# Kernel optimization log

Hardware: AMD Instinct MI355X
Metric: run time of the kernel (lower is better)

The kernel has to match this reference:

```python
import jax, jax.numpy as jnp
import numpy as np

B, C, H, W = 4, 256, 64, 64
EMB = C // 8  # embedding_channels = inChannels // k


def _conv1x1(x, w, b):
    # x: [B, Cin, H, W], w: [Cout, Cin], b: [Cout] -> [B, Cout, H, W]
    return jnp.einsum('oi,bihw->bohw', w, x) + b[None, :, None, None]


def setup_inputs() -> dict:
    key = jax.random.key(0)
    ks = jax.random.split(key, 10)
    s = 0.05
    return {
        'x': jax.random.normal(ks[0], (B, C, H, W), dtype=jnp.float32),
        'key_w': jax.random.normal(ks[1], (EMB, C), dtype=jnp.float32) * s,
        'key_b': jax.random.normal(ks[2], (EMB,), dtype=jnp.float32) * s,
        'query_w': jax.random.normal(ks[3], (EMB, C), dtype=jnp.float32) * s,
        'query_b': jax.random.normal(ks[4], (EMB,), dtype=jnp.float32) * s,
        'value_w': jax.random.normal(ks[5], (EMB, C), dtype=jnp.float32) * s,
        'value_b': jax.random.normal(ks[6], (EMB,), dtype=jnp.float32) * s,
        'att_w': jax.random.normal(ks[7], (C, EMB), dtype=jnp.float32) * s,
        'att_b': jax.random.normal(ks[8], (C,), dtype=jnp.float32) * s,
        'gamma': jnp.zeros((), dtype=jnp.float32),
    }


def reference(x, key_w, key_b, query_w, query_b, value_w, value_b, att_w, att_b, gamma):
    b, c, h, w = x.shape
    n = h * w
    f = _conv1x1(x, key_w, key_b).reshape(b, -1, n)    # [B, E, N]
    g = _conv1x1(x, query_w, query_b).reshape(b, -1, n)  # [B, E, N]
    hh = _conv1x1(x, value_w, value_b).reshape(b, -1, n)  # [B, E, N]
    # s[b,i,j] = sum_e f[b,e,i] * g[b,e,j]
    s = jnp.einsum('bei,bej->bij', f, g)  # [B, N, N]
    # NOTE: softmax over dim=1 (the i / key-index axis), NOT the last dim
    beta = jax.nn.softmax(s, axis=1)
    v = jnp.einsum('bei,bij->bej', hh, beta).reshape(b, -1, h, w)  # [B, E, H, W]
    o = _conv1x1(v, att_w, att_b)  # [B, C, H, W]
    y = gamma * o + x
    return (y, o)
```

## Files before the change

### kernel.cpp

```cpp
#include <hip/hip_runtime.h>
#include <hip/hip_bf16.h>
#include <math.h>

#define BB 4
#define CC 256
#define NN 4096
#define EE 32

typedef __attribute__((ext_vector_type(8))) short bf16x8;
typedef __attribute__((ext_vector_type(4))) float f32x4;
typedef __attribute__((ext_vector_type(16))) float f32x16;
typedef __attribute__((ext_vector_type(2))) unsigned uint32x2_t;

__device__ inline unsigned short f2bf(float x) {
    union { __hip_bfloat16 h; unsigned short u; } cv;
    cv.h = __float2bfloat16(x);
    return cv.u;
}
__device__ inline unsigned pk2(float lo, float hi) {
    return ((unsigned)f2bf(hi) << 16) | (unsigned)f2bf(lo);
}
__device__ inline float fexp2(float x) { return __builtin_amdgcn_exp2f(x); }
__device__ inline unsigned cvtpk(float lo, float hi) {
    unsigned r;
    asm("v_cvt_pk_bf16_f32 %0, %1, %2" : "=v"(r) : "v"(lo), "v"(hi));
    return r;
}
__device__ inline float bflo(unsigned u) {
    union { unsigned v; float f; } c; c.v = u << 16; return c.f;
}
__device__ inline float bfhi(unsigned u) {
    union { unsigned v; float f; } c; c.v = u & 0xFFFF0000u; return c.f;
}

__global__ __launch_bounds__(256) void wcvt_kernel(
    const float* __restrict__ kw, const float* __restrict__ kb,
    const float* __restrict__ qw, const float* __restrict__ qb,
    const float* __restrict__ vw, const float* __restrict__ vb,
    __hip_bfloat16* __restrict__ wB, float* __restrict__ bB)
{
    int r = blockIdx.x;
    int t = threadIdx.x;
    int rr = r & 31;
    const float* src; float scale = 1.f;
    if (r < 32)      src = kw;
    else if (r < 64) { src = qw; scale = 1.44269504f; }
    else             src = vw;
    if (t < 64) {
        float4 v = *(const float4*)(src + rr * 256 + t * 4);
        uint2 p;
        p.x = pk2(v.x * scale, v.y * scale);
        p.y = pk2(v.z * scale, v.w * scale);
        *(uint2*)((unsigned short*)wB + r * 256 + t * 4) = p;
    }
    if (r == 0 && t >= 64 && t < 160) {
        int e = t - 64;
        const float* bs = (e < 32) ? kb : ((e < 64) ? qb : vb);
        float sc = (e >= 32 && e < 64) ? 1.44269504f : 1.f;
        bB[e] = bs[e & 31] * sc;
    }
}

__global__ __launch_bounds__(256) void proj_kernel(
    const float* __restrict__ x,
    const __hip_bfloat16* __restrict__ wB, const float* __restrict__ bB,
    __hip_bfloat16* __restrict__ fT, __hip_bfloat16* __restrict__ gT,
    __hip_bfloat16* __restrict__ hT)
{
    __shared__ unsigned xs[32][132];
    int b     = blockIdx.x >> 7;
    int ibase = (blockIdx.x & 127) << 5;

    int t   = threadIdx.x;
    int ig4 = (t & 7) * 4;
    int crw = t >> 3;
    const float* xb = x + (size_t)b * CC * NN + ibase;
#pragma unroll
    for (int it = 0; it < 4; ++it) {
        int cp = it * 32 + crw;
        float4 fa = *(const float4*)(xb + (size_t)(2 * cp) * NN + ig4);
        float4 fc = *(const float4*)(xb + (size_t)(2 * cp + 1) * NN + ig4);
        xs[ig4 + 0][cp] = pk2(fa.x, fc.x);
        xs[ig4 + 1][cp] = pk2(fa.y, fc.y);
        xs[ig4 + 2][cp] = pk2(fa.z, fc.z);
        xs[ig4 + 3][cp] = pk2(fa.w, fc.w);
    }
    __syncthreads();

    int wv = threadIdx.x >> 6;
    int l  = threadIdx.x & 63;
    int q15  = l & 15, g = l >> 4;
    int isub = wv & 1, eh = wv >> 1;
    int irow = (isub << 4) + q15;
    const __hip_bfloat16* w0 = wB + ((size_t)(eh * 48) + q15) * 256;

    f32x4 a0 = {0,0,0,0}, a1 = {0,0,0,0}, a2 = {0,0,0,0};
#pragma unroll
    for (int kk = 0; kk < 8; ++kk) {
        bf16x8 Bf = *(const bf16x8*)&xs[irow][kk * 16 + 4 * g];
        int co = kk * 32 + 8 * g;
        bf16x8 A0 = *(const bf16x8*)(w0 + co);
        bf16x8 A1 = *(const bf16x8*)(w0 + 16 * 256 + co);
        bf16x8 A2 = *(const bf16x8*)(w0 + 32 * 256 + co);
        a0 = __builtin_amdgcn_mfma_f32_16x16x32_bf16(A0, Bf, a0, 0, 0, 0);
        a1 = __builtin_amdgcn_mfma_f32_16x16x32_bf16(A1, Bf, a1, 0, 0, 0);
        a2 = __builtin_amdgcn_mfma_f32_16x16x32_bf16(A2, Bf, a2, 0, 0, 0);
    }

    int ig = ibase + irow;
    auto emit = [&](f32x4 acc, int T) {
        float4 bb = *(const float4*)(bB + T * 16 + 4 * g);
        float d0 = acc[0] + bb.x, d1 = acc[1] + bb.y;
        float d2 = acc[2] + bb.z, d3 = acc[3] + bb.w;
        if (T < 4) {
            __hip_bfloat16* dst = (T < 2) ? fT : gT;
            int eoff = ((T & 1) << 4) + 4 * g;
            uint2 pq; pq.x = pk2(d0, d1); pq.y = pk2(d2, d3);
            *(uint2*)((unsigned short*)dst + ((size_t)b * NN + ig) * EE + eoff) = pq;
        } else {
            unsigned short* dst = (unsigned short*)hT;
            int e  = ((T - 4) << 4) + 4 * g;
            int kt = ig >> 5, kk2 = ig & 31;
            size_t base = ((size_t)(b * 128 + kt) * 32 + e) * 32 + kk2;
            dst[base]       = f2bf(d0);
            dst[base + 32]  = f2bf(d1);
            dst[base + 64]  = f2bf(d2);
            dst[base + 96]  = f2bf(d3);
        }
    };
    emit(a0, eh * 3 + 0);
    emit(a1, eh * 3 + 1);
    emit(a2, eh * 3 + 2);
}

__global__ __launch_bounds__(512, 4) void attn_kernel(
    const __hip_bfloat16* __restrict__ fT,
    const __hip_bfloat16* __restrict__ gT,
    const __hip_bfloat16* __restrict__ hT,
    unsigned short* __restrict__ part, float* __restrict__ lpart)
{
    int blk   = blockIdx.x;
    int b     = blk >> 7;
    int qt    = (blk >> 4) & 7;
    int kt    = blk & 15;
    int wv    = threadIdx.x >> 6;
    int lane  = threadIdx.x & 63;
    int q     = lane & 31;
    int h     = lane >> 5;
    int qbase = qt * 512 + wv * 64;

    const __hip_bfloat16* fb = fT + (size_t)b * NN * EE;
    const __hip_bfloat16* gb = gT + (size_t)b * NN * EE;
    const __hip_bfloat16* hb = hT + (size_t)b * NN * EE + q * 32 + 8 * h;

    bf16x8 Qa0 = *(const bf16x8*)(gb + (size_t)(qbase + q) * EE + 8 * h);
    bf16x8 Qa1 = *(const bf16x8*)(gb + (size_t)(qbase + q) * EE + 16 + 8 * h);
    bf16x8 Qb0 = *(const bf16x8*)(gb + (size_t)(qbase + 32 + q) * EE + 8 * h);
    bf16x8 Qb1 = *(const bf16x8*)(gb + (size_t)(qbase + 32 + q) * EE + 16 + 8 * h);

    float lA = 0.f, lB = 0.f;
    f32x16 OA = {0,0,0,0,0,0,0,0,0,0,0,0,0,0,0,0};
    f32x16 OB = {0,0,0,0,0,0,0,0,0,0,0,0,0,0,0,0};
    const f32x16 z16 = {0,0,0,0,0,0,0,0,0,0,0,0,0,0,0,0};

    int k0 = kt * 256;
    bf16x8 K0 = *(const bf16x8*)(fb + (size_t)(k0 + q) * EE + 8 * h);
    bf16x8 K1 = *(const bf16x8*)(fb + (size_t)(k0 + q) * EE + 16 + 8 * h);
    bf16x8 V0 = *(const bf16x8*)(hb + (size_t)k0 * 32);
    bf16x8 V1 = *(const bf16x8*)(hb + (size_t)k0 * 32 + 16);

    for (int c = 0; c < 8; ++c) {
        int kn = (k0 + 32) & (NN - 1);
        bf16x8 nK0 = *(const bf16x8*)(fb + (size_t)(kn + q) * EE + 8 * h);
        bf16x8 nK1 = *(const bf16x8*)(fb + (size_t)(kn + q) * EE + 16 + 8 * h);
        bf16x8 nV0 = *(const bf16x8*)(hb + (size_t)kn * 32);
        bf16x8 nV1 = *(const bf16x8*)(hb + (size_t)kn * 32 + 16);

        f32x16 SA0 = __builtin_amdgcn_mfma_f32_32x32x16_bf16(K0, Qa0, z16, 0, 0, 0);
        f32x16 SA1 = __builtin_amdgcn_mfma_f32_32x32x16_bf16(K1, Qa1, z16, 0, 0, 0);
        f32x16 SB0 = __builtin_amdgcn_mfma_f32_32x32x16_bf16(K0, Qb0, z16, 0, 0, 0);
        f32x16 SB1 = __builtin_amdgcn_mfma_f32_32x32x16_bf16(K1, Qb1, z16, 0, 0, 0);

        {
            float p[16];
#pragma unroll
            for (int r = 0; r < 16; ++r) p[r] = fexp2(SA0[r] + SA1[r]);
            lA += ((p[0]+p[1])+(p[2]+p[3])) + ((p[4]+p[5])+(p[6]+p[7]))
                + ((p[8]+p[9])+(p[10]+p[11])) + ((p[12]+p[13])+(p[14]+p[15]));
            unsigned j0 = cvtpk(p[0], p[1]),   j1 = cvtpk(p[2], p[3]);
            unsigned j2 = cvtpk(p[4], p[5]),   j3 = cvtpk(p[6], p[7]);
            unsigned j4 = cvtpk(p[8], p[9]),   j5 = cvtpk(p[10], p[11]);
            unsigned j6 = cvtpk(p[12], p[13]), j7 = cvtpk(p[14], p[15]);
            uint32x2_t sA2 = __builtin_amdgcn_permlane32_swap(j0, j2, false, false);
            uint32x2_t sB2 = __builtin_amdgcn_permlane32_swap(j1, j3, false, false);
            union { unsigned u[4]; bf16x8 v; } P1;
            P1.u[0] = sA2.x; P1.u[1] = sB2.x; P1.u[2] = sA2.y; P1.u[3] = sB2.y;
            uint32x2_t sC2 = __builtin_amdgcn_permlane32_swap(j4, j6, false, false);
            uint32x2_t sD2 = __builtin_amdgcn_permlane32_swap(j5, j7, false, false);
            union { unsigned u[4]; bf16x8 v; } P2;
            P2.u[0] = sC2.x; P2.u[1] = sD2.x; P2.u[2] = sC2.y; P2.u[3] = sD2.y;
            OA = __builtin_amdgcn_mfma_f32_32x32x16_bf16(V0, P1.v, OA, 0, 0, 0);
            OA = __builtin_amdgcn_mfma_f32_32x32x16_bf16(V1, P2.v, OA, 0, 0, 0);
        }

        {
            float p[16];
#pragma unroll
            for (int r = 0; r < 16; ++r) p[r] = fexp2(SB0[r] + SB1[r]);
            lB += ((p[0]+p[1])+(p[2]+p[3])) + ((p[4]+p[5])+(p[6]+p[7]))
                + ((p[8]+p[9])+(p[10]+p[11])) + ((p[12]+p[13])+(p[14]+p[15]));
            unsigned j0 = cvtpk(p[0], p[1]),   j1 = cvtpk(p[2], p[3]);
            unsigned j2 = cvtpk(p[4], p[5]),   j3 = cvtpk(p[6], p[7]);
            unsigned j4 = cvtpk(p[8], p[9]),   j5 = cvtpk(p[10], p[11]);
            unsigned j6 = cvtpk(p[12], p[13]), j7 = cvtpk(p[14], p[15]);
            uint32x2_t sA2 = __builtin_amdgcn_permlane32_swap(j0, j2, false, false);
            uint32x2_t sB2 = __builtin_amdgcn_permlane32_swap(j1, j3, false, false);
            union { unsigned u[4]; bf16x8 v; } P1;
            P1.u[0] = sA2.x; P1.u[1] = sB2.x; P1.u[2] = sA2.y; P1.u[3] = sB2.y;
            uint32x2_t sC2 = __builtin_amdgcn_permlane32_swap(j4, j6, false, false);
            uint32x2_t sD2 = __builtin_amdgcn_permlane32_swap(j5, j7, false, false);
            union { unsigned u[4]; bf16x8 v; } P2;
            P2.u[0] = sC2.x; P2.u[1] = sD2.x; P2.u[2] = sC2.y; P2.u[3] = sD2.y;
            OB = __builtin_amdgcn_mfma_f32_32x32x16_bf16(V0, P1.v, OB, 0, 0, 0);
            OB = __builtin_amdgcn_mfma_f32_32x32x16_bf16(V1, P2.v, OB, 0, 0, 0);
        }

        K0 = nK0; K1 = nK1; V0 = nV0; V1 = nV1;
        k0 = kn;
    }

    lA += __shfl_xor(lA, 32, 64);
    lB += __shfl_xor(lB, 32, 64);
    size_t pbase = (size_t)(b * 16 + kt) * NN;
    if (h == 0) {
        float* lp = lpart + pbase + qbase;
        lp[q]      = lA;
        lp[32 + q] = lB;
    }
    size_t oA = (pbase + qbase + q) * EE + 4 * h;
    size_t oB = (pbase + qbase + 32 + q) * EE + 4 * h;
#pragma unroll
    for (int gi = 0; gi < 4; ++gi) {
        uint2 pa, pb;
        pa.x = cvtpk(OA[4*gi],   OA[4*gi+1]);
        pa.y = cvtpk(OA[4*gi+2], OA[4*gi+3]);
        pb.x = cvtpk(OB[4*gi],   OB[4*gi+1]);
        pb.y = cvtpk(OB[4*gi+2], OB[4*gi+3]);
        *(uint2*)(part + oA + 8 * gi) = pa;
        *(uint2*)(part + oB + 8 * gi) = pb;
    }
}

__global__ __launch_bounds__(256) void reduce_kernel(
    const unsigned short* __restrict__ part, const float* __restrict__ lpart,
    float* __restrict__ vT)
{
    int blk = blockIdx.x;
    int b   = blk >> 6;
    int it  = blk & 63;
    int t   = threadIdx.x;
    int i   = it * 64 + (t >> 2);
    int g4  = t & 3;

    float l = 0.f;
    float acc[8];
#pragma unroll
    for (int r = 0; r < 8; ++r) acc[r] = 0.f;
#pragma unroll
    for (int kt = 0; kt < 16; ++kt) {
        size_t pbase = (size_t)(b * 16 + kt) * NN + i;
        l += lpart[pbase];
        uint4 u = *(const uint4*)(part + pbase * EE + g4 * 8);
        acc[0] += bflo(u.x); acc[1] += bfhi(u.x);
        acc[2] += bflo(u.y); acc[3] += bfhi(u.y);
        acc[4] += bflo(u.z); acc[5] += bfhi(u.z);
        acc[6] += bflo(u.w); acc[7] += bfhi(u.w);
    }
    float inv = 1.f / l;
    float* vp = vT + ((size_t)b * NN + i) * EE + g4 * 8;
    float4 o0 = make_float4(acc[0]*inv, acc[1]*inv, acc[2]*inv, acc[3]*inv);
    float4 o1 = make_float4(acc[4]*inv, acc[5]*inv, acc[6]*inv, acc[7]*inv);
    *(float4*)vp       = o0;
    *(float4*)(vp + 4) = o1;
}

__global__ __launch_bounds__(256) void out_kernel(
    const float* __restrict__ vT, const float* __restrict__ aw,
    const float* __restrict__ ab, const float* __restrict__ x,
    const float* __restrict__ gamma_p,
    float* __restrict__ y, float* __restrict__ o)
{
    int blk    = blockIdx.x;
    int csplit = blk & 15;
    int itile  = (blk >> 4) & 15;
    int b      = blk >> 8;
    int i      = itile * 256 + threadIdx.x;
    float gm   = gamma_p[0];

    const float4* vp4 = (const float4*)(vT + ((size_t)b * NN + i) * EE);
    float vr[EE];
#pragma unroll
    for (int u = 0; u < 8; ++u) {
        float4 t = vp4[u];
        vr[4*u+0] = t.x; vr[4*u+1] = t.y; vr[4*u+2] = t.z; vr[4*u+3] = t.w;
    }

    int co0 = csplit * 16;
#pragma unroll
    for (int co = co0; co < co0 + 16; ++co) {
        float s = ab[co];
#pragma unroll
        for (int e = 0; e < EE; ++e)
            s = fmaf(aw[co * EE + e], vr[e], s);
        size_t idx = ((size_t)b * CC + co) * NN + i;
        o[idx] = s;
        y[idx] = fmaf(gm, s, x[idx]);
    }
}

extern "C" void kernel_launch(void* const* d_in, const int* in_sizes, int n_in,
                              void* d_out, int out_size, void* d_ws, size_t ws_size,
                              hipStream_t stream)
{
    const float* x  = (const float*)d_in[0];
    const float* kw = (const float*)d_in[1];
    const float* kb = (const float*)d_in[2];
    const float* qw = (const float*)d_in[3];
    const float* qb = (const float*)d_in[4];
    const float* vw = (const float*)d_in[5];
    const float* vb = (const float*)d_in[6];
    const float* aw = (const float*)d_in[7];
    const float* ab = (const float*)d_in[8];
    const float* gm = (const float*)d_in[9];

    float* y = (float*)d_out;
    float* o = y + (size_t)BB * CC * NN;

    unsigned short* part  = (unsigned short*)d_ws;
    float*          lpart = (float*)(part + (size_t)BB * 16 * NN * EE);
    float*          vT    = lpart + (size_t)BB * 16 * NN;
    float*          bB    = vT + (size_t)BB * NN * EE;
    __hip_bfloat16* wB    = (__hip_bfloat16*)(bB + 128);
    __hip_bfloat16* fT    = wB + 96 * 256;
    __hip_bfloat16* gT    = fT + (size_t)BB * NN * EE;
    __hip_bfloat16* hT    = gT + (size_t)BB * NN * EE;

    wcvt_kernel<<<96, 256, 0, stream>>>(kw, kb, qw, qb, vw, vb, wB, bB);
    proj_kernel<<<BB * (NN / 32), 256, 0, stream>>>(x, wB, bB, fT, gT, hT);
    attn_kernel<<<BB * 8 * 16, 512, 0, stream>>>(fT, gT, hT, part, lpart);
    reduce_kernel<<<BB * 64, 256, 0, stream>>>(part, lpart, vT);
    out_kernel<<<BB * 16 * 16, 256, 0, stream>>>(vT, aw, ab, x, gm, y, o);
}
```

Measured before the change: 57.69 us.

## Halve per-wave query tile in attention kernel and double grid size

Each wave in the attention kernel now handles 32 queries instead of 64, and the grid doubles to 1024 blocks with launch bounds raised to 8 blocks per CU. The two score MFMAs now chain through the accumulator instead of being summed in VALU, and the V loads are no longer software-prefetched. The aim is more parallelism and lower register pressure for better occupancy and latency hiding. In exchange each K/V tile is loaded twice as often per query, and the exposed V load latency may stall the loop.

```diff
diff --git a/kernel.cpp b/kernel.cpp
--- a/kernel.cpp
+++ b/kernel.cpp
@@ -133,21 +133,21 @@
     emit(a2, eh * 3 + 2);
 }
 
-__global__ __launch_bounds__(512, 4) void attn_kernel(
+__global__ __launch_bounds__(512, 8) void attn_kernel(
     const __hip_bfloat16* __restrict__ fT,
     const __hip_bfloat16* __restrict__ gT,
     const __hip_bfloat16* __restrict__ hT,
     unsigned short* __restrict__ part, float* __restrict__ lpart)
 {
     int blk   = blockIdx.x;
-    int b     = blk >> 7;
-    int qt    = (blk >> 4) & 7;
+    int b     = blk >> 8;
+    int qt    = (blk >> 4) & 15;
     int kt    = blk & 15;
     int wv    = threadIdx.x >> 6;
     int lane  = threadIdx.x & 63;
     int q     = lane & 31;
     int h     = lane >> 5;
-    int qbase = qt * 512 + wv * 64;
+    int qbase = qt * 256 + wv * 32;
 
     const __hip_bfloat16* fb = fT + (size_t)b * NN * EE;
     const __hip_bfloat16* gb = gT + (size_t)b * NN * EE;
@@ -155,99 +155,64 @@
 
     bf16x8 Qa0 = *(const bf16x8*)(gb + (size_t)(qbase + q) * EE + 8 * h);
     bf16x8 Qa1 = *(const bf16x8*)(gb + (size_t)(qbase + q) * EE + 16 + 8 * h);
-    bf16x8 Qb0 = *(const bf16x8*)(gb + (size_t)(qbase + 32 + q) * EE + 8 * h);
-    bf16x8 Qb1 = *(const bf16x8*)(gb + (size_t)(qbase + 32 + q) * EE + 16 + 8 * h);
-
-    float lA = 0.f, lB = 0.f;
+
+    float lA = 0.f;
     f32x16 OA = {0,0,0,0,0,0,0,0,0,0,0,0,0,0,0,0};
-    f32x16 OB = {0,0,0,0,0,0,0,0,0,0,0,0,0,0,0,0};
     const f32x16 z16 = {0,0,0,0,0,0,0,0,0,0,0,0,0,0,0,0};
 
     int k0 = kt * 256;
     bf16x8 K0 = *(const bf16x8*)(fb + (size_t)(k0 + q) * EE + 8 * h);
     bf16x8 K1 = *(const bf16x8*)(fb + (size_t)(k0 + q) * EE + 16 + 8 * h);
-    bf16x8 V0 = *(const bf16x8*)(hb + (size_t)k0 * 32);
-    bf16x8 V1 = *(const bf16x8*)(hb + (size_t)k0 * 32 + 16);
 
     for (int c = 0; c < 8; ++c) {
         int kn = (k0 + 32) & (NN - 1);
         bf16x8 nK0 = *(const bf16x8*)(fb + (size_t)(kn + q) * EE + 8 * h);
         bf16x8 nK1 = *(const bf16x8*)(fb + (size_t)(kn + q) * EE + 16 + 8 * h);
-        bf16x8 nV0 = *(const bf16x8*)(hb + (size_t)kn * 32);
-        bf16x8 nV1 = *(const bf16x8*)(hb + (size_t)kn * 32 + 16);
-
-        f32x16 SA0 = __builtin_amdgcn_mfma_f32_32x32x16_bf16(K0, Qa0, z16, 0, 0, 0);
-        f32x16 SA1 = __builtin_amdgcn_mfma_f32_32x32x16_bf16(K1, Qa1, z16, 0, 0, 0);
-        f32x16 SB0 = __builtin_amdgcn_mfma_f32_32x32x16_bf16(K0, Qb0, z16, 0, 0, 0);
-        f32x16 SB1 = __builtin_amdgcn_mfma_f32_32x32x16_bf16(K1, Qb1, z16, 0, 0, 0);
-
-        {
-            float p[16];
-#pragma unroll
-            for (int r = 0; r < 16; ++r) p[r] = fexp2(SA0[r] + SA1[r]);
-            lA += ((p[0]+p[1])+(p[2]+p[3])) + ((p[4]+p[5])+(p[6]+p[7]))
-                + ((p[8]+p[9])+(p[10]+p[11])) + ((p[12]+p[13])+(p[14]+p[15]));
-            unsigned j0 = cvtpk(p[0], p[1]),   j1 = cvtpk(p[2], p[3]);
-            unsigned j2 = cvtpk(p[4], p[5]),   j3 = cvtpk(p[6], p[7]);
-            unsigned j4 = cvtpk(p[8], p[9]),   j5 = cvtpk(p[10], p[11]);
-            unsigned j6 = cvtpk(p[12], p[13]), j7 = cvtpk(p[14], p[15]);
-            uint32x2_t sA2 = __builtin_amdgcn_permlane32_swap(j0, j2, false, false);
-            uint32x2_t sB2 = __builtin_amdgcn_permlane32_swap(j1, j3, false, false);
-            union { unsigned u[4]; bf16x8 v; } P1;
-            P1.u[0] = sA2.x; P1.u[1] = sB2.x; P1.u[2] = sA2.y; P1.u[3] = sB2.y;
-            uint32x2_t sC2 = __builtin_amdgcn_permlane32_swap(j4, j6, false, false);
-            uint32x2_t sD2 = __builtin_amdgcn_permlane32_swap(j5, j7, false, false);
-            union { unsigned u[4]; bf16x8 v; } P2;
-            P2.u[0] = sC2.x; P2.u[1] = sD2.x; P2.u[2] = sC2.y; P2.u[3] = sD2.y;
-            OA = __builtin_amdgcn_mfma_f32_32x32x16_bf16(V0, P1.v, OA, 0, 0, 0);
-            OA = __builtin_amdgcn_mfma_f32_32x32x16_bf16(V1, P2.v, OA, 0, 0, 0);
-        }
-
-        {
-            float p[16];
-#pragma unroll
-            for (int r = 0; r < 16; ++r) p[r] = fexp2(SB0[r] + SB1[r]);
-            lB += ((p[0]+p[1])+(p[2]+p[3])) + ((p[4]+p[5])+(p[6]+p[7]))
-                + ((p[8]+p[9])+(p[10]+p[11])) + ((p[12]+p[13])+(p[14]+p[15]));
-            unsigned j0 = cvtpk(p[0], p[1]),   j1 = cvtpk(p[2], p[3]);
-            unsigned j2 = cvtpk(p[4], p[5]),   j3 = cvtpk(p[6], p[7]);
-            unsigned j4 = cvtpk(p[8], p[9]),   j5 = cvtpk(p[10], p[11]);
-            unsigned j6 = cvtpk(p[12], p[13]), j7 = cvtpk(p[14], p[15]);
-            uint32x2_t sA2 = __builtin_amdgcn_permlane32_swap(j0, j2, false, false);
-            uint32x2_t sB2 = __builtin_amdgcn_permlane32_swap(j1, j3, false, false);
-            union { unsigned u[4]; bf16x8 v; } P1;
-            P1.u[0] = sA2.x; P1.u[1] = sB2.x; P1.u[2] = sA2.y; P1.u[3] = sB2.y;
-            uint32x2_t sC2 = __builtin_amdgcn_permlane32_swap(j4, j6, false, false);
-            uint32x2_t sD2 = __builtin_amdgcn_permlane32_swap(j5, j7, false, false);
-            union { unsigned u[4]; bf16x8 v; } P2;
-            P2.u[0] = sC2.x; P2.u[1] = sD2.x; P2.u[2] = sC2.y; P2.u[3] = sD2.y;
-            OB = __builtin_amdgcn_mfma_f32_32x32x16_bf16(V0, P1.v, OB, 0, 0, 0);
-            OB = __builtin_amdgcn_mfma_f32_32x32x16_bf16(V1, P2.v, OB, 0, 0, 0);
-        }
-
-        K0 = nK0; K1 = nK1; V0 = nV0; V1 = nV1;
+        bf16x8 V0  = *(const bf16x8*)(hb + (size_t)k0 * 32);
+        bf16x8 V1  = *(const bf16x8*)(hb + (size_t)k0 * 32 + 16);
+
+        f32x16 SA = __builtin_amdgcn_mfma_f32_32x32x16_bf16(K0, Qa0, z16, 0, 0, 0);
+        SA = __builtin_amdgcn_mfma_f32_32x32x16_bf16(K1, Qa1, SA, 0, 0, 0);
+
+        float p[16];
+#pragma unroll
+        for (int r = 0; r < 16; ++r) p[r] = fexp2(SA[r]);
+        lA += ((p[0]+p[1])+(p[2]+p[3])) + ((p[4]+p[5])+(p[6]+p[7]))
+            + ((p[8]+p[9])+(p[10]+p[11])) + ((p[12]+p[13])+(p[14]+p[15]));
+
+        unsigned j0 = cvtpk(p[0], p[1]),   j1 = cvtpk(p[2], p[3]);
+        unsigned j2 = cvtpk(p[4], p[5]),   j3 = cvtpk(p[6], p[7]);
+        unsigned j4 = cvtpk(p[8], p[9]),   j5 = cvtpk(p[10], p[11]);
+        unsigned j6 = cvtpk(p[12], p[13]), j7 = cvtpk(p[14], p[15]);
+
+        uint32x2_t sA2 = __builtin_amdgcn_permlane32_swap(j0, j2, false, false);
+        uint32x2_t sB2 = __builtin_amdgcn_permlane32_swap(j1, j3, false, false);
+        union { unsigned u[4]; bf16x8 v; } P1;
+        P1.u[0] = sA2.x; P1.u[1] = sB2.x; P1.u[2] = sA2.y; P1.u[3] = sB2.y;
+        uint32x2_t sC2 = __builtin_amdgcn_permlane32_swap(j4, j6, false, false);
+        uint32x2_t sD2 = __builtin_amdgcn_permlane32_swap(j5, j7, false, false);
+        union { unsigned u[4]; bf16x8 v; } P2;
+        P2.u[0] = sC2.x; P2.u[1] = sD2.x; P2.u[2] = sC2.y; P2.u[3] = sD2.y;
+
+        OA = __builtin_amdgcn_mfma_f32_32x32x16_bf16(V0, P1.v, OA, 0, 0, 0);
+        OA = __builtin_amdgcn_mfma_f32_32x32x16_bf16(V1, P2.v, OA, 0, 0, 0);
+
+        K0 = nK0; K1 = nK1;
         k0 = kn;
     }
 
     lA += __shfl_xor(lA, 32, 64);
-    lB += __shfl_xor(lB, 32, 64);
     size_t pbase = (size_t)(b * 16 + kt) * NN;
     if (h == 0) {
-        float* lp = lpart + pbase + qbase;
-        lp[q]      = lA;
-        lp[32 + q] = lB;
+        lpart[pbase + qbase + q] = lA;
     }
     size_t oA = (pbase + qbase + q) * EE + 4 * h;
-    size_t oB = (pbase + qbase + 32 + q) * EE + 4 * h;
 #pragma unroll
     for (int gi = 0; gi < 4; ++gi) {
-        uint2 pa, pb;
+        uint2 pa;
         pa.x = cvtpk(OA[4*gi],   OA[4*gi+1]);
         pa.y = cvtpk(OA[4*gi+2], OA[4*gi+3]);
-        pb.x = cvtpk(OB[4*gi],   OB[4*gi+1]);
-        pb.y = cvtpk(OB[4*gi+2], OB[4*gi+3]);
         *(uint2*)(part + oA + 8 * gi) = pa;
-        *(uint2*)(part + oB + 8 * gi) = pb;
     }
 }
 
@@ -347,7 +312,7 @@
 
     wcvt_kernel<<<96, 256, 0, stream>>>(kw, kb, qw, qb, vw, vb, wB, bB);
     proj_kernel<<<BB * (NN / 32), 256, 0, stream>>>(x, wB, bB, fT, gT, hT);
-    attn_kernel<<<BB * 8 * 16, 512, 0, stream>>>(fT, gT, hT, part, lpart);
+    attn_kernel<<<BB * 16 * 16, 512, 0, stream>>>(fT, gT, hT, part, lpart);
     reduce_kernel<<<BB * 64, 256, 0, stream>>>(part, lpart, vT);
     out_kernel<<<BB * 16 * 16, 256, 0, stream>>>(vT, aw, ab, x, gm, y, o);
 }
```

Result: slower. 62.54 us (+8.4%).
